# Kernel optimization log

Hardware: AMD Instinct MI355X
Metric: run time of the kernel (lower is better)

The kernel has to match this reference:

```python
import jax, jax.numpy as jnp
import numpy as np

E = 768   # embed_size
H = 64    # head_embed_size
B = 8
T = 4096  # == ctx_size


def setup_inputs() -> dict:
    key = jax.random.key(0)
    k1, k2, k3, k4 = jax.random.split(key, 4)
    inputs = jax.random.normal(k1, (B, T, E), dtype=jnp.float32)
    # Linear weights stored as (E, H) so projection is x @ W
    scale = 1.0 / np.sqrt(E)
    Wq = jax.random.uniform(k2, (E, H), dtype=jnp.float32, minval=-scale, maxval=scale)
    Wk = jax.random.uniform(k3, (E, H), dtype=jnp.float32, minval=-scale, maxval=scale)
    Wv = jax.random.uniform(k4, (E, H), dtype=jnp.float32, minval=-scale, maxval=scale)
    return {"inputs": inputs, "Wq": Wq, "Wk": Wk, "Wv": Wv}


def reference(inputs, Wq, Wk, Wv):
    Tlen = inputs.shape[1]
    q = inputs @ Wq  # (B,T,H)
    k = inputs @ Wk  # (B,T,H)
    v = inputs @ Wv  # (B,T,H)
    # NOTE: original module does NOT scale by 1/sqrt(H) — faithful reproduction.
    scores = jnp.einsum('bqh,bkh->bqk', q, k)  # (B,T,T)
    causal = jnp.tril(jnp.ones((Tlen, Tlen), dtype=bool))
    scores = jnp.where(causal, scores, -jnp.inf)
    attn = jax.nn.softmax(scores, axis=-1)
    # dropout=0 -> identity
    out = jnp.einsum('bqk,bkh->bqh', attn, v)  # (B,T,H)
    return out
```

## Files before the change

kernel.cpp:

```cpp
#include <hip/hip_runtime.h>
#include <hip/hip_bf16.h>

#define E_DIM 768
#define H_DIM 64
#define B_SZ 8
#define T_SZ 4096
#define BT (B_SZ * T_SZ)

typedef __attribute__((ext_vector_type(8))) short short8;
typedef __attribute__((ext_vector_type(4))) float floatx4;

#define RAWBAR() __asm__ volatile("s_waitcnt lgkmcnt(0)\n\ts_barrier" ::: "memory")

static __device__ __forceinline__ unsigned short bf1(float a) {
    __hip_bfloat16 h = __float2bfloat16(a);
    unsigned short u; __builtin_memcpy(&u, &h, 2); return u;
}
static __device__ __forceinline__ unsigned int pk2(float a, float b) {
    __hip_bfloat162 h = __float22bfloat162_rn(float2{a, b});
    unsigned int u; __builtin_memcpy(&u, &h, 4); return u;
}

__global__ __launch_bounds__(256) void prep_w(
    const float* __restrict__ Wq, const float* __restrict__ Wk,
    const float* __restrict__ Wv, unsigned short* __restrict__ Wt)
{
    __shared__ float Ls[64][65];
    const int nt = blockIdx.x;
    const int kc = blockIdx.y;
    const float* __restrict__ W = (nt == 0) ? Wq : (nt == 1) ? Wk : Wv;
    const int t = threadIdx.x;
    const int k0 = kc * 64;

#pragma unroll
    for (int it = 0; it < 16; ++it) {
        const int kk = (t >> 6) + it * 4;
        Ls[kk][t & 63] = W[(size_t)(k0 + kk) * H_DIM + (t & 63)];
    }
    __syncthreads();

#pragma unroll
    for (int it = 0; it < 4; ++it) {
        const int nl = (t >> 4) + it * 16;
        const int kl = (t & 15) * 4;
        unsigned int u[2];
        u[0] = pk2(Ls[kl + 0][nl], Ls[kl + 1][nl]);
        u[1] = pk2(Ls[kl + 2][nl], Ls[kl + 3][nl]);
        *(uint2*)(Wt + (size_t)(nt * 64 + nl) * E_DIM + k0 + kl) = *(uint2*)u;
    }
}

__global__ __launch_bounds__(768) void proj_mfma(
    const float* __restrict__ X, const unsigned short* __restrict__ Wt,
    unsigned short* __restrict__ Qb, unsigned short* __restrict__ Kb,
    unsigned short* __restrict__ Vtb)
{
    __shared__ unsigned short Xs[2][16][776];

    const int tid  = threadIdx.x;
    const int wave = tid >> 6, lane = tid & 63;
    const int row  = lane & 15, quad = lane >> 4;
    const int m0   = blockIdx.x * 128;

    short8 bfr[24];
    {
        const unsigned short* wp = Wt + (size_t)(wave * 16 + row) * E_DIM + quad * 8;
#pragma unroll
        for (int ks = 0; ks < 24; ++ks) bfr[ks] = *(const short8*)(wp + ks * 32);
    }

    const int srow = tid & 15;
    const int sc   = tid >> 4;
    const float* __restrict__ xbase = X + (size_t)(m0 + srow) * E_DIM + sc * 16;

    float4 fx[4];
#define LDX(mt)                                                               \
    {                                                                         \
        const float* p = xbase + (size_t)(mt) * 16 * E_DIM;                   \
        fx[0] = *(const float4*)(p);     fx[1] = *(const float4*)(p + 4);     \
        fx[2] = *(const float4*)(p + 8); fx[3] = *(const float4*)(p + 12);    \
    }
#define STX(buf)                                                              \
    {                                                                         \
        unsigned int tmp[8];                                                  \
        tmp[0] = pk2(fx[0].x, fx[0].y); tmp[1] = pk2(fx[0].z, fx[0].w);       \
        tmp[2] = pk2(fx[1].x, fx[1].y); tmp[3] = pk2(fx[1].z, fx[1].w);       \
        tmp[4] = pk2(fx[2].x, fx[2].y); tmp[5] = pk2(fx[2].z, fx[2].w);       \
        tmp[6] = pk2(fx[3].x, fx[3].y); tmp[7] = pk2(fx[3].z, fx[3].w);       \
        *(int4*)&Xs[buf][srow][sc * 16]     = *(int4*)&tmp[0];                \
        *(int4*)&Xs[buf][srow][sc * 16 + 8] = *(int4*)&tmp[4];                \
    }

    LDX(0); STX(0);
    RAWBAR();

    const int g  = wave >> 2;
    const int h  = (wave & 3) * 16 + row;
    unsigned short* __restrict__ OQK = (g == 0) ? Qb : Kb;
    const int bb = m0 >> 12;

    int cur = 0;
    for (int mt = 0; mt < 8; ++mt) {
        if (mt < 7) LDX(mt + 1);

        floatx4 acc = (floatx4)0.0f;
#pragma unroll
        for (int ks = 0; ks < 24; ++ks) {
            const short8 af = *(const short8*)&Xs[cur][row][ks * 32 + quad * 8];
            acc = __builtin_amdgcn_mfma_f32_16x16x32_bf16(af, bfr[ks], acc, 0, 0, 0);
        }

        const int mr = m0 + mt * 16 + quad * 4;
        if (g < 2) {
#pragma unroll
            for (int r = 0; r < 4; ++r)
                OQK[(size_t)(mr + r) * H_DIM + h] = bf1(acc[r]);
        } else {
            const int t0 = mr & 4095;
            unsigned int u[2];
            u[0] = pk2(acc[0], acc[1]); u[1] = pk2(acc[2], acc[3]);
            *(uint2*)(Vtb + ((size_t)bb * H_DIM + h) * T_SZ + t0) = *(uint2*)u;
        }

        if (mt < 7) STX(cur ^ 1);
        RAWBAR();
        cur ^= 1;
    }
#undef LDX
#undef STX
}

typedef unsigned short KVrow[72];

__global__ __launch_bounds__(256) void attn_mfma(
    const unsigned short* __restrict__ Qb,
    const unsigned short* __restrict__ Kb,
    const unsigned short* __restrict__ Vtb,
    float* __restrict__ Out)
{
    __shared__ unsigned short Ks[3][64][72];
    __shared__ unsigned short Vs[3][64][72];
    __shared__ unsigned short Ps[4][16][76];

    const int lb   = blockIdx.x;
    const int b    = lb & 7;
    const int qt   = 63 - (lb >> 3);
    const int tid  = threadIdx.x;
    const int wave = tid >> 6, lane = tid & 63;
    const int row  = lane & 15, quad = lane >> 4;

    const size_t base = (size_t)b * T_SZ * H_DIM;
    const int q0 = qt * 64 + wave * 16;

    const int krow = tid >> 2, kcol = (tid & 3) * 16;
    const unsigned short* __restrict__ Ksrc = Kb + base + (size_t)krow * H_DIM + kcol;
    const int vh = tid >> 2, vseg = (tid & 3) * 16;
    const unsigned short* __restrict__ Vsrc = Vtb + ((size_t)b * H_DIM + vh) * T_SZ + vseg;

    short8 qf0, qf1;
    {
        const unsigned short* qp = Qb + base + (size_t)(q0 + row) * H_DIM + quad * 8;
        qf0 = *(const short8*)(qp);
        qf1 = *(const short8*)(qp + 32);
    }

    floatx4 o[4];
#pragma unroll
    for (int i = 0; i < 4; ++i) o[i] = (floatx4)0.0f;
    float lp[4] = {0.0f, 0.0f, 0.0f, 0.0f};

    KVrow* kp0 = Ks[0]; KVrow* kp1 = Ks[1]; KVrow* kp2 = Ks[2];
    KVrow* vp0 = Vs[0]; KVrow* vp1 = Vs[1]; KVrow* vp2 = Vs[2];

    int4 kA0, kA1, vA0, vA1, kB0, kB1, vB0, vB1;

#define LDKV(K0, K1, V0, V1, t)                                          \
    {                                                                    \
        const unsigned short* kp = Ksrc + (size_t)(t) * 64 * H_DIM;      \
        K0 = *(const int4*)kp; K1 = *(const int4*)(kp + 8);              \
        const unsigned short* vp = Vsrc + (t) * 64;                      \
        V0 = *(const int4*)vp; V1 = *(const int4*)(vp + 8);              \
    }
#define STKV(K0, K1, V0, V1, KD, VD)                                     \
    {                                                                    \
        *(int4*)&KD[krow][kcol] = K0; *(int4*)&KD[krow][kcol + 8] = K1;  \
        *(int4*)&VD[vh][vseg]   = V0; *(int4*)&VD[vh][vseg + 8]   = V1;  \
    }
#define ROTATE()                                                         \
    { KVrow* tk = kp0; kp0 = kp1; kp1 = kp2; kp2 = tk;                   \
      KVrow* tv = vp0; vp0 = vp1; vp1 = vp2; vp2 = tv; }

    auto compute = [&](int t, KVrow* kc, KVrow* vc) {
        floatx4 s[4];
#pragma unroll
        for (int nt = 0; nt < 4; ++nt) {
            const unsigned short* kp = &kc[nt * 16 + row][quad * 8];
            floatx4 a = (floatx4)0.0f;
            a = __builtin_amdgcn_mfma_f32_16x16x32_bf16(qf0, *(const short8*)(kp),      a, 0, 0, 0);
            a = __builtin_amdgcn_mfma_f32_16x16x32_bf16(qf1, *(const short8*)(kp + 32), a, 0, 0, 0);
            s[nt] = a;
        }
        if (t == qt) {
#pragma unroll
            for (int nt = 0; nt < 4; ++nt) {
                const int key_loc = nt * 16 + row;
#pragma unroll
                for (int r = 0; r < 4; ++r)
                    if (key_loc > wave * 16 + quad * 4 + r) s[nt][r] = -1e30f;
            }
        }
#pragma unroll
        for (int r = 0; r < 4; ++r) {
#pragma unroll
            for (int nt = 0; nt < 4; ++nt) {
                const float pv = __expf(fminf(s[nt][r], 80.0f));
                lp[r] += pv;
                Ps[wave][quad * 4 + r][nt * 16 + row] = bf1(pv);
            }
        }
        __builtin_amdgcn_wave_barrier();
#pragma unroll
        for (int kst = 0; kst < 2; ++kst) {
            const short8 pa = *(const short8*)(&Ps[wave][row][kst * 32 + quad * 8]);
#pragma unroll
            for (int nt = 0; nt < 4; ++nt) {
                const short8 vb = *(const short8*)(&vc[nt * 16 + row][kst * 32 + quad * 8]);
                o[nt] = __builtin_amdgcn_mfma_f32_16x16x32_bf16(pa, vb, o[nt], 0, 0, 0);
            }
        }
    };

    LDKV(kA0, kA1, vA0, vA1, 0);
    STKV(kA0, kA1, vA0, vA1, kp0, vp0);
    if (qt >= 1) LDKV(kB0, kB1, vB0, vB1, 1);
    RAWBAR();

    int kt = 0;
    while (true) {
        if (kt + 2 <= qt) LDKV(kA0, kA1, vA0, vA1, kt + 2);
        if (kt + 1 <= qt) STKV(kB0, kB1, vB0, vB1, kp1, vp1);
        compute(kt, kp0, vp0);
        RAWBAR();
        ROTATE();
        ++kt;
        if (kt > qt) break;

        if (kt + 2 <= qt) LDKV(kB0, kB1, vB0, vB1, kt + 2);
        if (kt + 1 <= qt) STKV(kA0, kA1, vA0, vA1, kp1, vp1);
        compute(kt, kp0, vp0);
        RAWBAR();
        ROTATE();
        ++kt;
        if (kt > qt) break;
    }

#pragma unroll
    for (int r = 0; r < 4; ++r) {
        float l = lp[r];
#pragma unroll
        for (int off = 1; off < 16; off <<= 1)
            l += __shfl_xor(l, off, 16);
        const float inv = 1.0f / l;
        float* op = Out + base + (size_t)(q0 + quad * 4 + r) * H_DIM + row;
#pragma unroll
        for (int nt = 0; nt < 4; ++nt)
            op[nt * 16] = o[nt][r] * inv;
    }
#undef LDKV
#undef STKV
#undef ROTATE
}

extern "C" void kernel_launch(void* const* d_in, const int* in_sizes, int n_in,
                              void* d_out, int out_size, void* d_ws, size_t ws_size,
                              hipStream_t stream) {
    const float* X  = (const float*)d_in[0];
    const float* Wq = (const float*)d_in[1];
    const float* Wk = (const float*)d_in[2];
    const float* Wv = (const float*)d_in[3];

    unsigned short* Wt  = (unsigned short*)d_ws;
    unsigned short* Qb  = Wt + (size_t)192 * E_DIM;
    unsigned short* Kb  = Qb + (size_t)BT * H_DIM;
    unsigned short* Vtb = Kb + (size_t)BT * H_DIM;

    prep_w<<<dim3(3, 12), 256, 0, stream>>>(Wq, Wk, Wv, Wt);
    proj_mfma<<<256, 768, 0, stream>>>(X, Wt, Qb, Kb, Vtb);
    attn_mfma<<<512, 256, 0, stream>>>(Qb, Kb, Vtb, (float*)d_out);
}
```

Baseline: 237.9 us.

## Load K fragments directly from global, fold log2e into Wq, widen projection tiles

In the attention kernel, K is no longer staged through shared memory. Each wave reads its MFMA K fragments straight from global/L2, which removes the K LDS stores and cuts LDS use, and occupancy hints are added. Wq is prescaled by log2(e) so the softmax can use exp2f instead of __expf. The projection kernel now processes 32-row tiles with two accumulators and gets a 3-block occupancy hint. The costs are redundant global K reads across the four waves, rounding from prescaling Q before bf16, and higher register pressure in the projection kernel.

After: 299.3 us. +25.8%, slower.

```diff
diff --git a/kernel.cpp b/kernel.cpp
--- a/kernel.cpp
+++ b/kernel.cpp
@@ -29,6 +29,7 @@
     const int nt = blockIdx.x;
     const int kc = blockIdx.y;
     const float* __restrict__ W = (nt == 0) ? Wq : (nt == 1) ? Wk : Wv;
+    const float scl = (nt == 0) ? 1.44269504088896f : 1.0f;
     const int t = threadIdx.x;
     const int k0 = kc * 64;
 
@@ -44,18 +45,18 @@
         const int nl = (t >> 4) + it * 16;
         const int kl = (t & 15) * 4;
         unsigned int u[2];
-        u[0] = pk2(Ls[kl + 0][nl], Ls[kl + 1][nl]);
-        u[1] = pk2(Ls[kl + 2][nl], Ls[kl + 3][nl]);
+        u[0] = pk2(Ls[kl + 0][nl] * scl, Ls[kl + 1][nl] * scl);
+        u[1] = pk2(Ls[kl + 2][nl] * scl, Ls[kl + 3][nl] * scl);
         *(uint2*)(Wt + (size_t)(nt * 64 + nl) * E_DIM + k0 + kl) = *(uint2*)u;
     }
 }
 
-__global__ __launch_bounds__(768) void proj_mfma(
+__global__ __launch_bounds__(768, 3) void proj_mfma(
     const float* __restrict__ X, const unsigned short* __restrict__ Wt,
     unsigned short* __restrict__ Qb, unsigned short* __restrict__ Kb,
     unsigned short* __restrict__ Vtb)
 {
-    __shared__ unsigned short Xs[2][16][776];
+    __shared__ unsigned short Xs[2][32][776];
 
     const int tid  = threadIdx.x;
     const int wave = tid >> 6, lane = tid & 63;
@@ -69,26 +70,28 @@
         for (int ks = 0; ks < 24; ++ks) bfr[ks] = *(const short8*)(wp + ks * 32);
     }
 
-    const int srow = tid & 15;
-    const int sc   = tid >> 4;
-    const float* __restrict__ xbase = X + (size_t)(m0 + srow) * E_DIM + sc * 16;
-
-    float4 fx[4];
+    const int srow = tid & 31;
+    const int sc   = tid >> 5;
+    const float* __restrict__ xbase = X + (size_t)(m0 + srow) * E_DIM + sc * 32;
+
+    float4 fx[8];
 #define LDX(mt)                                                               \
     {                                                                         \
-        const float* p = xbase + (size_t)(mt) * 16 * E_DIM;                   \
-        fx[0] = *(const float4*)(p);     fx[1] = *(const float4*)(p + 4);     \
-        fx[2] = *(const float4*)(p + 8); fx[3] = *(const float4*)(p + 12);    \
+        const float* p = xbase + (size_t)(mt) * 32 * E_DIM;                   \
+        _Pragma("unroll")                                                     \
+        for (int i = 0; i < 8; ++i) fx[i] = *(const float4*)(p + i * 4);      \
     }
 #define STX(buf)                                                              \
     {                                                                         \
-        unsigned int tmp[8];                                                  \
-        tmp[0] = pk2(fx[0].x, fx[0].y); tmp[1] = pk2(fx[0].z, fx[0].w);       \
-        tmp[2] = pk2(fx[1].x, fx[1].y); tmp[3] = pk2(fx[1].z, fx[1].w);       \
-        tmp[4] = pk2(fx[2].x, fx[2].y); tmp[5] = pk2(fx[2].z, fx[2].w);       \
-        tmp[6] = pk2(fx[3].x, fx[3].y); tmp[7] = pk2(fx[3].z, fx[3].w);       \
-        *(int4*)&Xs[buf][srow][sc * 16]     = *(int4*)&tmp[0];                \
-        *(int4*)&Xs[buf][srow][sc * 16 + 8] = *(int4*)&tmp[4];                \
+        unsigned int tmp[16];                                                 \
+        _Pragma("unroll")                                                     \
+        for (int i = 0; i < 8; ++i) {                                         \
+            tmp[2 * i]     = pk2(fx[i].x, fx[i].y);                           \
+            tmp[2 * i + 1] = pk2(fx[i].z, fx[i].w);                           \
+        }                                                                     \
+        _Pragma("unroll")                                                     \
+        for (int i = 0; i < 4; ++i)                                           \
+            *(int4*)&Xs[buf][srow][sc * 32 + i * 8] = *(int4*)&tmp[4 * i];    \
     }
 
     LDX(0); STX(0);
@@ -100,29 +103,35 @@
     const int bb = m0 >> 12;
 
     int cur = 0;
-    for (int mt = 0; mt < 8; ++mt) {
-        if (mt < 7) LDX(mt + 1);
-
-        floatx4 acc = (floatx4)0.0f;
+    for (int mt = 0; mt < 4; ++mt) {
+        if (mt < 3) LDX(mt + 1);
+
+        floatx4 acc[2] = {(floatx4)0.0f, (floatx4)0.0f};
 #pragma unroll
         for (int ks = 0; ks < 24; ++ks) {
-            const short8 af = *(const short8*)&Xs[cur][row][ks * 32 + quad * 8];
-            acc = __builtin_amdgcn_mfma_f32_16x16x32_bf16(af, bfr[ks], acc, 0, 0, 0);
-        }
-
-        const int mr = m0 + mt * 16 + quad * 4;
-        if (g < 2) {
-#pragma unroll
-            for (int r = 0; r < 4; ++r)
-                OQK[(size_t)(mr + r) * H_DIM + h] = bf1(acc[r]);
-        } else {
-            const int t0 = mr & 4095;
-            unsigned int u[2];
-            u[0] = pk2(acc[0], acc[1]); u[1] = pk2(acc[2], acc[3]);
-            *(uint2*)(Vtb + ((size_t)bb * H_DIM + h) * T_SZ + t0) = *(uint2*)u;
-        }
-
-        if (mt < 7) STX(cur ^ 1);
+#pragma unroll
+            for (int ms = 0; ms < 2; ++ms) {
+                const short8 af = *(const short8*)&Xs[cur][ms * 16 + row][ks * 32 + quad * 8];
+                acc[ms] = __builtin_amdgcn_mfma_f32_16x16x32_bf16(af, bfr[ks], acc[ms], 0, 0, 0);
+            }
+        }
+
+#pragma unroll
+        for (int ms = 0; ms < 2; ++ms) {
+            const int mr = m0 + mt * 32 + ms * 16 + quad * 4;
+            if (g < 2) {
+#pragma unroll
+                for (int r = 0; r < 4; ++r)
+                    OQK[(size_t)(mr + r) * H_DIM + h] = bf1(acc[ms][r]);
+            } else {
+                const int t0 = mr & 4095;
+                unsigned int u[2];
+                u[0] = pk2(acc[ms][0], acc[ms][1]); u[1] = pk2(acc[ms][2], acc[ms][3]);
+                *(uint2*)(Vtb + ((size_t)bb * H_DIM + h) * T_SZ + t0) = *(uint2*)u;
+            }
+        }
+
+        if (mt < 3) STX(cur ^ 1);
         RAWBAR();
         cur ^= 1;
     }
@@ -132,13 +141,12 @@
 
 typedef unsigned short KVrow[72];
 
-__global__ __launch_bounds__(256) void attn_mfma(
+__global__ __launch_bounds__(256, 4) void attn_mfma(
     const unsigned short* __restrict__ Qb,
     const unsigned short* __restrict__ Kb,
     const unsigned short* __restrict__ Vtb,
     float* __restrict__ Out)
 {
-    __shared__ unsigned short Ks[3][64][72];
     __shared__ unsigned short Vs[3][64][72];
     __shared__ unsigned short Ps[4][16][76];
 
@@ -152,10 +160,9 @@
     const size_t base = (size_t)b * T_SZ * H_DIM;
     const int q0 = qt * 64 + wave * 16;
 
-    const int krow = tid >> 2, kcol = (tid & 3) * 16;
-    const unsigned short* __restrict__ Ksrc = Kb + base + (size_t)krow * H_DIM + kcol;
     const int vh = tid >> 2, vseg = (tid & 3) * 16;
     const unsigned short* __restrict__ Vsrc = Vtb + ((size_t)b * H_DIM + vh) * T_SZ + vseg;
+    const unsigned short* __restrict__ Kfrag = Kb + base + (size_t)row * H_DIM + quad * 8;
 
     short8 qf0, qf1;
     {
@@ -169,35 +176,29 @@
     for (int i = 0; i < 4; ++i) o[i] = (floatx4)0.0f;
     float lp[4] = {0.0f, 0.0f, 0.0f, 0.0f};
 
-    KVrow* kp0 = Ks[0]; KVrow* kp1 = Ks[1]; KVrow* kp2 = Ks[2];
     KVrow* vp0 = Vs[0]; KVrow* vp1 = Vs[1]; KVrow* vp2 = Vs[2];
-
-    int4 kA0, kA1, vA0, vA1, kB0, kB1, vB0, vB1;
-
-#define LDKV(K0, K1, V0, V1, t)                                          \
+    int4 vA0, vA1, vB0, vB1;
+
+#define LDV(V0, V1, t)                                                   \
     {                                                                    \
-        const unsigned short* kp = Ksrc + (size_t)(t) * 64 * H_DIM;      \
-        K0 = *(const int4*)kp; K1 = *(const int4*)(kp + 8);              \
         const unsigned short* vp = Vsrc + (t) * 64;                      \
         V0 = *(const int4*)vp; V1 = *(const int4*)(vp + 8);              \
     }
-#define STKV(K0, K1, V0, V1, KD, VD)                                     \
-    {                                                                    \
-        *(int4*)&KD[krow][kcol] = K0; *(int4*)&KD[krow][kcol + 8] = K1;  \
-        *(int4*)&VD[vh][vseg]   = V0; *(int4*)&VD[vh][vseg + 8]   = V1;  \
-    }
+#define STV(V0, V1, VD)                                                  \
+    { *(int4*)&VD[vh][vseg] = V0; *(int4*)&VD[vh][vseg + 8] = V1; }
 #define ROTATE()                                                         \
-    { KVrow* tk = kp0; kp0 = kp1; kp1 = kp2; kp2 = tk;                   \
-      KVrow* tv = vp0; vp0 = vp1; vp1 = vp2; vp2 = tv; }
-
-    auto compute = [&](int t, KVrow* kc, KVrow* vc) {
+    { KVrow* tv = vp0; vp0 = vp1; vp1 = vp2; vp2 = tv; }
+
+    auto compute = [&](int t, KVrow* vc) {
+        const unsigned short* kp = Kfrag + (size_t)t * 64 * H_DIM;
         floatx4 s[4];
 #pragma unroll
         for (int nt = 0; nt < 4; ++nt) {
-            const unsigned short* kp = &kc[nt * 16 + row][quad * 8];
+            const short8 kf0 = *(const short8*)(kp + nt * 16 * H_DIM);
+            const short8 kf1 = *(const short8*)(kp + nt * 16 * H_DIM + 32);
             floatx4 a = (floatx4)0.0f;
-            a = __builtin_amdgcn_mfma_f32_16x16x32_bf16(qf0, *(const short8*)(kp),      a, 0, 0, 0);
-            a = __builtin_amdgcn_mfma_f32_16x16x32_bf16(qf1, *(const short8*)(kp + 32), a, 0, 0, 0);
+            a = __builtin_amdgcn_mfma_f32_16x16x32_bf16(qf0, kf0, a, 0, 0, 0);
+            a = __builtin_amdgcn_mfma_f32_16x16x32_bf16(qf1, kf1, a, 0, 0, 0);
             s[nt] = a;
         }
         if (t == qt) {
@@ -213,7 +214,7 @@
         for (int r = 0; r < 4; ++r) {
 #pragma unroll
             for (int nt = 0; nt < 4; ++nt) {
-                const float pv = __expf(fminf(s[nt][r], 80.0f));
+                const float pv = exp2f(fminf(s[nt][r], 110.0f));
                 lp[r] += pv;
                 Ps[wave][quad * 4 + r][nt * 16 + row] = bf1(pv);
             }
@@ -230,24 +231,24 @@
         }
     };
 
-    LDKV(kA0, kA1, vA0, vA1, 0);
-    STKV(kA0, kA1, vA0, vA1, kp0, vp0);
-    if (qt >= 1) LDKV(kB0, kB1, vB0, vB1, 1);
+    LDV(vA0, vA1, 0);
+    STV(vA0, vA1, vp0);
+    if (qt >= 1) LDV(vB0, vB1, 1);
     RAWBAR();
 
     int kt = 0;
     while (true) {
-        if (kt + 2 <= qt) LDKV(kA0, kA1, vA0, vA1, kt + 2);
-        if (kt + 1 <= qt) STKV(kB0, kB1, vB0, vB1, kp1, vp1);
-        compute(kt, kp0, vp0);
+        if (kt + 2 <= qt) LDV(vA0, vA1, kt + 2);
+        if (kt + 1 <= qt) STV(vB0, vB1, vp1);
+        compute(kt, vp0);
         RAWBAR();
         ROTATE();
         ++kt;
         if (kt > qt) break;
 
-        if (kt + 2 <= qt) LDKV(kB0, kB1, vB0, vB1, kt + 2);
-        if (kt + 1 <= qt) STKV(kA0, kA1, vA0, vA1, kp1, vp1);
-        compute(kt, kp0, vp0);
+        if (kt + 2 <= qt) LDV(vB0, vB1, kt + 2);
+        if (kt + 1 <= qt) STV(vA0, vA1, vp1);
+        compute(kt, vp0);
         RAWBAR();
         ROTATE();
         ++kt;
@@ -266,8 +267,8 @@
         for (int nt = 0; nt < 4; ++nt)
             op[nt * 16] = o[nt][r] * inv;
     }
-#undef LDKV
-#undef STKV
+#undef LDV
+#undef STV
 #undef ROTATE
 }
 
```
